# Kernel tuning notes

Measured on AMD Instinct MI355X. Metric: run time of the kernel, lower is better.

Reference implementation:

```python
import jax, jax.numpy as jnp
import numpy as np

D_MODEL = 1024
N_HEADS = 16
HEAD_DIM = D_MODEL // N_HEADS
L = 2048


def setup_inputs() -> dict:
    key = jax.random.key(0)
    ks = jax.random.split(key, 7)
    x = jax.random.normal(ks[0], (L, D_MODEL), dtype=jnp.float32)
    pair_bias = jax.random.normal(ks[1], (N_HEADS, L, L), dtype=jnp.float32)
    gate = jax.random.uniform(ks[2], (N_HEADS, 1, 1), dtype=jnp.float32)
    # Learned params (Linear stores weight [out, in]; y = x @ W.T + b)
    s_qkv = 1.0 / np.sqrt(D_MODEL)
    W_qkv = jax.random.uniform(ks[3], (3 * D_MODEL, D_MODEL), minval=-s_qkv, maxval=s_qkv, dtype=jnp.float32)
    b_qkv = jax.random.uniform(ks[4], (3 * D_MODEL,), minval=-s_qkv, maxval=s_qkv, dtype=jnp.float32)
    W_out = jax.random.uniform(ks[5], (D_MODEL, D_MODEL), minval=-s_qkv, maxval=s_qkv, dtype=jnp.float32)
    b_out = jax.random.uniform(ks[6], (D_MODEL,), minval=-s_qkv, maxval=s_qkv, dtype=jnp.float32)
    return {"x": x, "pair_bias": pair_bias, "gate": gate,
            "W_qkv": W_qkv, "b_qkv": b_qkv, "W_out": W_out, "b_out": b_out}


def reference(x, pair_bias, gate, W_qkv, b_qkv, W_out, b_out):
    Lx = x.shape[0]
    scale = HEAD_DIM ** -0.5
    qkv = (x @ W_qkv.T + b_qkv).reshape(Lx, 3, N_HEADS, HEAD_DIM)
    q, k, v = qkv[:, 0], qkv[:, 1], qkv[:, 2]  # [L, H, Dh]
    logits = jnp.einsum('ihd,jhd->hij', q, k) * scale + gate * pair_bias
    attn = jax.nn.softmax(logits, axis=-1)  # dropout p=0 (eval) -> identity
    out = jnp.einsum('hij,jhd->ihd', attn, v).reshape(Lx, D_MODEL)
    return out @ W_out.T + b_out
```

## Files before the change

### kernel.cpp

```cpp
#include <hip/hip_runtime.h>
#include <cstdint>
#include <cstddef>

#define L_SEQ  2048
#define DMODEL 1024
#define NHEADS 16
#define HDIM   64
#define NQKV   3072

typedef float f32x4 __attribute__((ext_vector_type(4)));
typedef short s16x8 __attribute__((ext_vector_type(8)));

static __device__ __forceinline__ unsigned short f2bf(float f) {
  unsigned u = __float_as_uint(f);
  return (unsigned short)((u + 0x7fffu + ((u >> 16) & 1u)) >> 16);
}

static __device__ __forceinline__ void gld_lds16(void* lds, const void* g) {
  __builtin_amdgcn_global_load_lds(
      (const __attribute__((address_space(1))) void*)g,
      (__attribute__((address_space(3))) void*)lds, 16, 0, 0);
}

__global__ __launch_bounds__(256) void cvt_kernel(
    const float* __restrict__ x, const float* __restrict__ wqkv,
    const float* __restrict__ wout,
    unsigned short* __restrict__ xb, unsigned short* __restrict__ wqkvb,
    unsigned short* __restrict__ woutb) {
  const int NX = L_SEQ * DMODEL / 4;
  const int NW1 = NQKV * DMODEL / 4;
  const int NW2 = DMODEL * DMODEL / 4;
  const int tot = NX + NW1 + NW2;
  for (int i = blockIdx.x * blockDim.x + threadIdx.x; i < tot;
       i += gridDim.x * blockDim.x) {
    const float4* s;
    unsigned short* d;
    int j;
    if (i < NX) { s = (const float4*)x; d = xb; j = i; }
    else if (i < NX + NW1) { s = (const float4*)wqkv; d = wqkvb; j = i - NX; }
    else { s = (const float4*)wout; d = woutb; j = i - NX - NW1; }
    float4 v = s[j];
    ushort4 o;
    o.x = f2bf(v.x); o.y = f2bf(v.y); o.z = f2bf(v.z); o.w = f2bf(v.w);
    *(ushort4*)(d + 4 * (size_t)j) = o;
  }
}

template <int KDIM>
static __device__ __forceinline__ void gemm_bt_core(
    const unsigned short* __restrict__ A, const unsigned short* __restrict__ Bt,
    unsigned short* As, unsigned short* Bs, int bm, int bn, f32x4 acc[4][4]) {
  const int tid = threadIdx.x;
  const int lane = tid & 63;
  const int wave = tid >> 6;
  const int g = lane >> 4;
  const int li = lane & 15;
  const int wm = (wave >> 1) * 64;
  const int wn = (wave & 1) * 64;
  const int arow = tid >> 2;
  const int acolb = (tid & 3) << 4;
  const char* gA = (const char*)A + (size_t)(bm * 128 + arow) * (KDIM * 2) + acolb;
  const char* gB = (const char*)Bt + (size_t)(bn * 128 + arow) * (KDIM * 2) + acolb;
  char* lA = (char*)As + wave * 1024;
  char* lB = (char*)Bs + wave * 1024;
  const size_t half = (size_t)64 * KDIM * 2;
  for (int kt = 0; kt < KDIM; kt += 32) {
    __syncthreads();
    gld_lds16(lA, gA + kt * 2);
    gld_lds16(lA + 4096, gA + half + kt * 2);
    gld_lds16(lB, gB + kt * 2);
    gld_lds16(lB + 4096, gB + half + kt * 2);
    __syncthreads();
    const s16x8* Av = (const s16x8*)As;
    const s16x8* Bv = (const s16x8*)Bs;
    s16x8 af[4], bfv[4];
#pragma unroll
    for (int mt = 0; mt < 4; ++mt) af[mt] = Av[(wm + mt * 16 + li) * 4 + g];
#pragma unroll
    for (int nt = 0; nt < 4; ++nt) bfv[nt] = Bv[(wn + nt * 16 + li) * 4 + g];
#pragma unroll
    for (int mt = 0; mt < 4; ++mt)
#pragma unroll
      for (int nt = 0; nt < 4; ++nt)
        acc[mt][nt] = __builtin_amdgcn_mfma_f32_16x16x32_bf16(
            af[mt], bfv[nt], acc[mt][nt], 0, 0, 0);
  }
}

__global__ __launch_bounds__(256, 2) void gemm_qkv_k(
    const unsigned short* __restrict__ A, const unsigned short* __restrict__ Bt,
    const float* __restrict__ bqkv, unsigned short* __restrict__ Qb,
    unsigned short* __restrict__ Kb, unsigned short* __restrict__ Vt) {
  __shared__ alignas(16) unsigned short As[128 * 32], Bs[128 * 32];
  f32x4 acc[4][4] = {};
  gemm_bt_core<DMODEL>(A, Bt, As, Bs, blockIdx.x, blockIdx.y, acc);
  const int lane = threadIdx.x & 63, wave = threadIdx.x >> 6;
  const int g = lane >> 4, li = lane & 15;
  const int wm = (wave >> 1) * 64, wn = (wave & 1) * 64;
#pragma unroll
  for (int mt = 0; mt < 4; ++mt)
#pragma unroll
    for (int nt = 0; nt < 4; ++nt)
#pragma unroll
      for (int r = 0; r < 4; ++r) {
        int i = blockIdx.x * 128 + wm + mt * 16 + 4 * g + r;
        int n = blockIdx.y * 128 + wn + nt * 16 + li;
        float v = acc[mt][nt][r] + bqkv[n];
        int s = n >> 10;
        int h = (n >> 6) & 15;
        int d = n & 63;
        if (s == 0)      Qb[(((size_t)h * L_SEQ + i) << 6) + d] = f2bf(v * 0.125f);
        else if (s == 1) Kb[(((size_t)h * L_SEQ + i) << 6) + d] = f2bf(v);
        else             Vt[(size_t)(h * 64 + d) * L_SEQ + i] = f2bf(v);
      }
}

__global__ __launch_bounds__(256, 4) void attn_k(
    const unsigned short* __restrict__ Qb, const unsigned short* __restrict__ Kb,
    const unsigned short* __restrict__ Vt, const float* __restrict__ bias,
    const float* __restrict__ gate, unsigned short* __restrict__ AO) {
  __shared__ alignas(16) char lds[16 * 1024 + 256];
  const int h = blockIdx.y;
  const int tid = threadIdx.x, lane = tid & 63, wave = tid >> 6;
  const int g = lane >> 4, li = lane & 15;
  const int i0 = blockIdx.x * 16;
  char* myP = lds + wave * 2048;
  const s16x8* Qv = (const s16x8*)(Qb + (((size_t)h * L_SEQ + i0) << 6));
  const s16x8 qf0 = Qv[li * 8 + g];
  const s16x8 qf1 = Qv[li * 8 + 4 + g];
  const float gh = gate[h];
  const float* bh = bias + (size_t)h * L_SEQ * L_SEQ + (size_t)i0 * L_SEQ;
  f32x4 accO[4] = {};
  f32x4 lpart = {0.f, 0.f, 0.f, 0.f};

  for (int t = 0; t < 8; ++t) {
    const int j0 = t * 256 + wave * 64;
    const s16x8* Kv = (const s16x8*)(Kb + (((size_t)h * L_SEQ + j0) << 6));
    s16x8 k0[4], k1[4];
#pragma unroll
    for (int nt = 0; nt < 4; ++nt) {
      k0[nt] = Kv[(nt * 16 + li) * 8 + g];
      k1[nt] = Kv[(nt * 16 + li) * 8 + 4 + g];
    }
    float bv[4][4];
#pragma unroll
    for (int r = 0; r < 4; ++r)
#pragma unroll
      for (int nt = 0; nt < 4; ++nt)
        bv[r][nt] = bh[(size_t)(4 * g + r) * L_SEQ + j0 + nt * 16 + li];
    f32x4 s[4];
#pragma unroll
    for (int nt = 0; nt < 4; ++nt) {
      f32x4 z = {0.f, 0.f, 0.f, 0.f};
      z = __builtin_amdgcn_mfma_f32_16x16x32_bf16(qf0, k0[nt], z, 0, 0, 0);
      z = __builtin_amdgcn_mfma_f32_16x16x32_bf16(qf1, k1[nt], z, 0, 0, 0);
      s[nt] = z;
    }
#pragma unroll
    for (int nt = 0; nt < 4; ++nt)
#pragma unroll
      for (int r = 0; r < 4; ++r) {
        float p = __expf(fmaf(gh, bv[r][nt], s[nt][r]));
        lpart[r] += p;
        int row = 4 * g + r, col = nt * 16 + li;
        unsigned b = (unsigned)(row * 128 + col * 2) ^ (unsigned)((row & 7) << 4);
        *(unsigned short*)(myP + b) = f2bf(p);
      }
    asm volatile("s_waitcnt lgkmcnt(0)" ::: "memory");
    unsigned b0 = ((unsigned)(li * 128 + 16 * g)) ^ (unsigned)((li & 7) << 4);
    unsigned b1 = ((unsigned)(li * 128 + 64 + 16 * g)) ^ (unsigned)((li & 7) << 4);
    s16x8 pa0 = *(const s16x8*)(myP + b0);
    s16x8 pa1 = *(const s16x8*)(myP + b1);
#pragma unroll
    for (int dt = 0; dt < 4; ++dt) {
      size_t vb = (size_t)(h * 64 + dt * 16 + li) * L_SEQ + j0;
      s16x8 v0 = *(const s16x8*)(Vt + vb + 8 * g);
      s16x8 v1 = *(const s16x8*)(Vt + vb + 32 + 8 * g);
      accO[dt] = __builtin_amdgcn_mfma_f32_16x16x32_bf16(pa0, v0, accO[dt], 0, 0, 0);
      accO[dt] = __builtin_amdgcn_mfma_f32_16x16x32_bf16(pa1, v1, accO[dt], 0, 0, 0);
    }
  }
  float lrow[4];
#pragma unroll
  for (int r = 0; r < 4; ++r) {
    float tl = lpart[r];
    tl += __shfl_xor(tl, 1);
    tl += __shfl_xor(tl, 2);
    tl += __shfl_xor(tl, 4);
    tl += __shfl_xor(tl, 8);
    lrow[r] = tl;
  }
  __syncthreads();
  float* accL = (float*)lds;
  float* lL = (float*)(lds + 16 * 1024);
#pragma unroll
  for (int dt = 0; dt < 4; ++dt)
#pragma unroll
    for (int r = 0; r < 4; ++r)
      accL[(wave * 16 + 4 * g + r) * 64 + dt * 16 + li] = accO[dt][r];
  if (li == 0) {
#pragma unroll
    for (int r = 0; r < 4; ++r) lL[wave * 16 + 4 * g + r] = lrow[r];
  }
  __syncthreads();
  {
    const int row = tid >> 4;
    const int c0 = (tid & 15) * 4;
    f32x4 sum = {0.f, 0.f, 0.f, 0.f};
    float lsum = 0.f;
#pragma unroll
    for (int w = 0; w < 4; ++w) {
      const f32x4 a = *(const f32x4*)&accL[(w * 16 + row) * 64 + c0];
      sum += a;
      lsum += lL[w * 16 + row];
    }
    const float inv = 1.0f / lsum;
    ushort4 o;
    o.x = f2bf(sum[0] * inv);
    o.y = f2bf(sum[1] * inv);
    o.z = f2bf(sum[2] * inv);
    o.w = f2bf(sum[3] * inv);
    *(ushort4*)(AO + (size_t)(i0 + row) * DMODEL + h * 64 + c0) = o;
  }
}

__global__ __launch_bounds__(256, 2) void gemm_out_k(
    const unsigned short* __restrict__ A, const unsigned short* __restrict__ Bt,
    const float* __restrict__ bout, float* __restrict__ out) {
  __shared__ alignas(16) unsigned short As[128 * 32], Bs[128 * 32];
  f32x4 acc[4][4] = {};
  gemm_bt_core<DMODEL>(A, Bt, As, Bs, blockIdx.x, blockIdx.y, acc);
  const int lane = threadIdx.x & 63, wave = threadIdx.x >> 6;
  const int g = lane >> 4, li = lane & 15;
  const int wm = (wave >> 1) * 64, wn = (wave & 1) * 64;
#pragma unroll
  for (int mt = 0; mt < 4; ++mt)
#pragma unroll
    for (int nt = 0; nt < 4; ++nt)
#pragma unroll
      for (int r = 0; r < 4; ++r) {
        int i = blockIdx.x * 128 + wm + mt * 16 + 4 * g + r;
        int n = blockIdx.y * 128 + wn + nt * 16 + li;
        out[(size_t)i * DMODEL + n] = acc[mt][nt][r] + bout[n];
      }
}

extern "C" void kernel_launch(void* const* d_in, const int* in_sizes, int n_in,
                              void* d_out, int out_size, void* d_ws,
                              size_t ws_size, hipStream_t stream) {
  const float* x = (const float*)d_in[0];
  const float* pb = (const float*)d_in[1];
  const float* gate = (const float*)d_in[2];
  const float* wqkv = (const float*)d_in[3];
  const float* bqkv = (const float*)d_in[4];
  const float* wout = (const float*)d_in[5];
  const float* bout = (const float*)d_in[6];

  unsigned short* ws = (unsigned short*)d_ws;
  unsigned short* xb = ws;
  unsigned short* wqkvb = xb + (size_t)L_SEQ * DMODEL;
  unsigned short* woutb = wqkvb + (size_t)NQKV * DMODEL;
  unsigned short* Qb = woutb + (size_t)DMODEL * DMODEL;
  unsigned short* Kb = Qb + (size_t)NHEADS * L_SEQ * HDIM;
  unsigned short* Vt = Kb + (size_t)NHEADS * L_SEQ * HDIM;
  unsigned short* AO = Vt + (size_t)NHEADS * L_SEQ * HDIM;

  cvt_kernel<<<1024, 256, 0, stream>>>(x, wqkv, wout, xb, wqkvb, woutb);
  gemm_qkv_k<<<dim3(16, 24), 256, 0, stream>>>(xb, wqkvb, bqkv, Qb, Kb, Vt);
  attn_k<<<dim3(128, 16), 256, 0, stream>>>(Qb, Kb, Vt, pb, gate, AO);
  gemm_out_k<<<dim3(16, 8), 256, 0, stream>>>(AO, woutb, bout, (float*)d_out);
}
```

Before: 204.6 us.

## Software-pipeline K and bias loads in attention loop with register double buffering

Prefetches the next iteration's K fragments and pair-bias values into double-buffered registers while the current tile computes, and hoists V loads to the top of each iteration. The aim is to hide global-memory latency on the bias stream, which dominates traffic. The loop is fully unrolled and occupancy is lowered from 4 to 2 blocks per SIMD in launch bounds to make room for the extra registers. That trades latency hiding through more waves for latency hiding through explicit prefetch.

```diff
diff --git a/kernel.cpp b/kernel.cpp
--- a/kernel.cpp
+++ b/kernel.cpp
@@ -115,7 +115,7 @@
       }
 }
 
-__global__ __launch_bounds__(256, 4) void attn_k(
+__global__ __launch_bounds__(256, 2) void attn_k(
     const unsigned short* __restrict__ Qb, const unsigned short* __restrict__ Kb,
     const unsigned short* __restrict__ Vt, const float* __restrict__ bias,
     const float* __restrict__ gate, unsigned short* __restrict__ AO) {
@@ -130,37 +130,68 @@
   const s16x8 qf1 = Qv[li * 8 + 4 + g];
   const float gh = gate[h];
   const float* bh = bias + (size_t)h * L_SEQ * L_SEQ + (size_t)i0 * L_SEQ;
+  const s16x8* Kall = (const s16x8*)(Kb + (((size_t)h * L_SEQ) << 6));
   f32x4 accO[4] = {};
   f32x4 lpart = {0.f, 0.f, 0.f, 0.f};
 
+  s16x8 kf[2][8];
+  float bb[2][16];
+
+  {
+    const int j0 = wave * 64;
+#pragma unroll
+    for (int nt = 0; nt < 4; ++nt) {
+      kf[0][2 * nt] = Kall[(j0 + nt * 16 + li) * 8 + g];
+      kf[0][2 * nt + 1] = Kall[(j0 + nt * 16 + li) * 8 + 4 + g];
+    }
+#pragma unroll
+    for (int r = 0; r < 4; ++r)
+#pragma unroll
+      for (int nt = 0; nt < 4; ++nt)
+        bb[0][4 * r + nt] = bh[(size_t)(4 * g + r) * L_SEQ + j0 + nt * 16 + li];
+  }
+
+#pragma unroll
   for (int t = 0; t < 8; ++t) {
+    const int cb = t & 1, nb = cb ^ 1;
     const int j0 = t * 256 + wave * 64;
-    const s16x8* Kv = (const s16x8*)(Kb + (((size_t)h * L_SEQ + j0) << 6));
-    s16x8 k0[4], k1[4];
-#pragma unroll
-    for (int nt = 0; nt < 4; ++nt) {
-      k0[nt] = Kv[(nt * 16 + li) * 8 + g];
-      k1[nt] = Kv[(nt * 16 + li) * 8 + 4 + g];
-    }
-    float bv[4][4];
-#pragma unroll
-    for (int r = 0; r < 4; ++r)
-#pragma unroll
-      for (int nt = 0; nt < 4; ++nt)
-        bv[r][nt] = bh[(size_t)(4 * g + r) * L_SEQ + j0 + nt * 16 + li];
+    s16x8 v0[4], v1[4];
+#pragma unroll
+    for (int dt = 0; dt < 4; ++dt) {
+      const unsigned short* vb = Vt + (size_t)(h * 64 + dt * 16 + li) * L_SEQ + j0;
+      v0[dt] = *(const s16x8*)(vb + 8 * g);
+      v1[dt] = *(const s16x8*)(vb + 32 + 8 * g);
+    }
+    if (t < 7) {
+      const int jn = j0 + 256;
+#pragma unroll
+      for (int r = 0; r < 4; ++r)
+#pragma unroll
+        for (int nt = 0; nt < 4; ++nt)
+          bb[nb][4 * r + nt] =
+              bh[(size_t)(4 * g + r) * L_SEQ + jn + nt * 16 + li];
+    }
     f32x4 s[4];
 #pragma unroll
     for (int nt = 0; nt < 4; ++nt) {
       f32x4 z = {0.f, 0.f, 0.f, 0.f};
-      z = __builtin_amdgcn_mfma_f32_16x16x32_bf16(qf0, k0[nt], z, 0, 0, 0);
-      z = __builtin_amdgcn_mfma_f32_16x16x32_bf16(qf1, k1[nt], z, 0, 0, 0);
+      z = __builtin_amdgcn_mfma_f32_16x16x32_bf16(qf0, kf[cb][2 * nt], z, 0, 0, 0);
+      z = __builtin_amdgcn_mfma_f32_16x16x32_bf16(qf1, kf[cb][2 * nt + 1], z, 0, 0, 0);
       s[nt] = z;
     }
+    if (t < 7) {
+      const int jn = j0 + 256;
+#pragma unroll
+      for (int nt = 0; nt < 4; ++nt) {
+        kf[nb][2 * nt] = Kall[(jn + nt * 16 + li) * 8 + g];
+        kf[nb][2 * nt + 1] = Kall[(jn + nt * 16 + li) * 8 + 4 + g];
+      }
+    }
 #pragma unroll
     for (int nt = 0; nt < 4; ++nt)
 #pragma unroll
       for (int r = 0; r < 4; ++r) {
-        float p = __expf(fmaf(gh, bv[r][nt], s[nt][r]));
+        float p = __expf(fmaf(gh, bb[cb][4 * r + nt], s[nt][r]));
         lpart[r] += p;
         int row = 4 * g + r, col = nt * 16 + li;
         unsigned b = (unsigned)(row * 128 + col * 2) ^ (unsigned)((row & 7) << 4);
@@ -173,11 +204,8 @@
     s16x8 pa1 = *(const s16x8*)(myP + b1);
 #pragma unroll
     for (int dt = 0; dt < 4; ++dt) {
-      size_t vb = (size_t)(h * 64 + dt * 16 + li) * L_SEQ + j0;
-      s16x8 v0 = *(const s16x8*)(Vt + vb + 8 * g);
-      s16x8 v1 = *(const s16x8*)(Vt + vb + 32 + 8 * g);
-      accO[dt] = __builtin_amdgcn_mfma_f32_16x16x32_bf16(pa0, v0, accO[dt], 0, 0, 0);
-      accO[dt] = __builtin_amdgcn_mfma_f32_16x16x32_bf16(pa1, v1, accO[dt], 0, 0, 0);
+      accO[dt] = __builtin_amdgcn_mfma_f32_16x16x32_bf16(pa0, v0[dt], accO[dt], 0, 0, 0);
+      accO[dt] = __builtin_amdgcn_mfma_f32_16x16x32_bf16(pa1, v1[dt], accO[dt], 0, 0, 0);
     }
   }
   float lrow[4];
```

Result: faster. 191.0 us (-6.7%).

## Split attention into score kernel writing exp scores and separate PV kernel

Applied to the files above, without the earlier changes.

Splits the fused attention kernel into two. The first computes exp(QK^T + gate*bias) for every tile in parallel across a 3D grid and stores bf16 probabilities to a global buffer. The second reads those probabilities, sums them for normalization, and multiplies them by V. This exposes more parallelism for the bias-streaming stage but adds a large global round trip of the full score matrix and needs extra workspace.

```diff
diff --git a/kernel.cpp b/kernel.cpp
--- a/kernel.cpp
+++ b/kernel.cpp
@@ -14,6 +14,10 @@
 static __device__ __forceinline__ unsigned short f2bf(float f) {
   unsigned u = __float_as_uint(f);
   return (unsigned short)((u + 0x7fffu + ((u >> 16) & 1u)) >> 16);
+}
+
+static __device__ __forceinline__ float bf2f(unsigned short u) {
+  return __uint_as_float(((unsigned)u) << 16);
 }
 
 static __device__ __forceinline__ void gld_lds16(void* lds, const void* g) {
@@ -115,82 +119,92 @@
       }
 }
 
-__global__ __launch_bounds__(256, 4) void attn_k(
+__global__ __launch_bounds__(256) void attn_score_k(
     const unsigned short* __restrict__ Qb, const unsigned short* __restrict__ Kb,
-    const unsigned short* __restrict__ Vt, const float* __restrict__ bias,
-    const float* __restrict__ gate, unsigned short* __restrict__ AO) {
-  __shared__ alignas(16) char lds[16 * 1024 + 256];
-  const int h = blockIdx.y;
+    const float* __restrict__ bias, const float* __restrict__ gate,
+    unsigned short* __restrict__ E) {
+  __shared__ alignas(16) char plds[4 * 2048];
+  const int h = blockIdx.z;
+  const int i0 = blockIdx.x * 16;
   const int tid = threadIdx.x, lane = tid & 63, wave = tid >> 6;
   const int g = lane >> 4, li = lane & 15;
-  const int i0 = blockIdx.x * 16;
-  char* myP = lds + wave * 2048;
+  const int j0 = blockIdx.y * 256 + wave * 64;
+  char* myP = plds + wave * 2048;
   const s16x8* Qv = (const s16x8*)(Qb + (((size_t)h * L_SEQ + i0) << 6));
   const s16x8 qf0 = Qv[li * 8 + g];
   const s16x8 qf1 = Qv[li * 8 + 4 + g];
   const float gh = gate[h];
-  const float* bh = bias + (size_t)h * L_SEQ * L_SEQ + (size_t)i0 * L_SEQ;
+  const float* bh = bias + (size_t)h * L_SEQ * L_SEQ + (size_t)i0 * L_SEQ + j0;
+  const s16x8* Kv = (const s16x8*)(Kb + (((size_t)h * L_SEQ + j0) << 6));
+  s16x8 k0[4], k1[4];
+#pragma unroll
+  for (int nt = 0; nt < 4; ++nt) {
+    k0[nt] = Kv[(nt * 16 + li) * 8 + g];
+    k1[nt] = Kv[(nt * 16 + li) * 8 + 4 + g];
+  }
+  float bv[4][4];
+#pragma unroll
+  for (int r = 0; r < 4; ++r)
+#pragma unroll
+    for (int nt = 0; nt < 4; ++nt)
+      bv[r][nt] = bh[(size_t)(4 * g + r) * L_SEQ + nt * 16 + li];
+  f32x4 s[4];
+#pragma unroll
+  for (int nt = 0; nt < 4; ++nt) {
+    f32x4 z = {0.f, 0.f, 0.f, 0.f};
+    z = __builtin_amdgcn_mfma_f32_16x16x32_bf16(qf0, k0[nt], z, 0, 0, 0);
+    z = __builtin_amdgcn_mfma_f32_16x16x32_bf16(qf1, k1[nt], z, 0, 0, 0);
+    s[nt] = z;
+  }
+#pragma unroll
+  for (int nt = 0; nt < 4; ++nt)
+#pragma unroll
+    for (int r = 0; r < 4; ++r) {
+      float p = __expf(fmaf(gh, bv[r][nt], s[nt][r]));
+      const int row = 4 * g + r, col = nt * 16 + li;
+      unsigned b = (unsigned)(row * 128 + col * 2) ^ (unsigned)((row & 7) << 4);
+      *(unsigned short*)(myP + b) = f2bf(p);
+    }
+  asm volatile("s_waitcnt lgkmcnt(0)" ::: "memory");
+  const unsigned b0 = ((unsigned)(li * 128 + 16 * g)) ^ (unsigned)((li & 7) << 4);
+  const unsigned b1 = ((unsigned)(li * 128 + 64 + 16 * g)) ^ (unsigned)((li & 7) << 4);
+  const s16x8 pa0 = *(const s16x8*)(myP + b0);
+  const s16x8 pa1 = *(const s16x8*)(myP + b1);
+  unsigned short* Eo = E + ((size_t)h * L_SEQ + (i0 + li)) * L_SEQ + j0 + 8 * g;
+  *(s16x8*)Eo = pa0;
+  *(s16x8*)(Eo + 32) = pa1;
+}
+
+__global__ __launch_bounds__(256) void attn_pv_k(
+    const unsigned short* __restrict__ E, const unsigned short* __restrict__ Vt,
+    unsigned short* __restrict__ AO) {
+  __shared__ alignas(16) char lds[16 * 1024 + 256];
+  const int h = blockIdx.y;
+  const int tid = threadIdx.x, lane = tid & 63, wave = tid >> 6;
+  const int g = lane >> 4, li = lane & 15;
+  const int i0 = blockIdx.x * 16;
+  const unsigned short* Eb = E + ((size_t)h * L_SEQ + (i0 + li)) * L_SEQ;
   f32x4 accO[4] = {};
-  f32x4 lpart = {0.f, 0.f, 0.f, 0.f};
-
+  float lsum = 0.f;
+#pragma unroll
   for (int t = 0; t < 8; ++t) {
     const int j0 = t * 256 + wave * 64;
-    const s16x8* Kv = (const s16x8*)(Kb + (((size_t)h * L_SEQ + j0) << 6));
-    s16x8 k0[4], k1[4];
-#pragma unroll
-    for (int nt = 0; nt < 4; ++nt) {
-      k0[nt] = Kv[(nt * 16 + li) * 8 + g];
-      k1[nt] = Kv[(nt * 16 + li) * 8 + 4 + g];
-    }
-    float bv[4][4];
-#pragma unroll
-    for (int r = 0; r < 4; ++r)
-#pragma unroll
-      for (int nt = 0; nt < 4; ++nt)
-        bv[r][nt] = bh[(size_t)(4 * g + r) * L_SEQ + j0 + nt * 16 + li];
-    f32x4 s[4];
-#pragma unroll
-    for (int nt = 0; nt < 4; ++nt) {
-      f32x4 z = {0.f, 0.f, 0.f, 0.f};
-      z = __builtin_amdgcn_mfma_f32_16x16x32_bf16(qf0, k0[nt], z, 0, 0, 0);
-      z = __builtin_amdgcn_mfma_f32_16x16x32_bf16(qf1, k1[nt], z, 0, 0, 0);
-      s[nt] = z;
-    }
-#pragma unroll
-    for (int nt = 0; nt < 4; ++nt)
-#pragma unroll
-      for (int r = 0; r < 4; ++r) {
-        float p = __expf(fmaf(gh, bv[r][nt], s[nt][r]));
-        lpart[r] += p;
-        int row = 4 * g + r, col = nt * 16 + li;
-        unsigned b = (unsigned)(row * 128 + col * 2) ^ (unsigned)((row & 7) << 4);
-        *(unsigned short*)(myP + b) = f2bf(p);
-      }
-    asm volatile("s_waitcnt lgkmcnt(0)" ::: "memory");
-    unsigned b0 = ((unsigned)(li * 128 + 16 * g)) ^ (unsigned)((li & 7) << 4);
-    unsigned b1 = ((unsigned)(li * 128 + 64 + 16 * g)) ^ (unsigned)((li & 7) << 4);
-    s16x8 pa0 = *(const s16x8*)(myP + b0);
-    s16x8 pa1 = *(const s16x8*)(myP + b1);
+    const s16x8 pa0 = *(const s16x8*)(Eb + j0 + 8 * g);
+    const s16x8 pa1 = *(const s16x8*)(Eb + j0 + 32 + 8 * g);
+#pragma unroll
+    for (int e = 0; e < 8; ++e)
+      lsum += bf2f((unsigned short)pa0[e]) + bf2f((unsigned short)pa1[e]);
 #pragma unroll
     for (int dt = 0; dt < 4; ++dt) {
-      size_t vb = (size_t)(h * 64 + dt * 16 + li) * L_SEQ + j0;
-      s16x8 v0 = *(const s16x8*)(Vt + vb + 8 * g);
-      s16x8 v1 = *(const s16x8*)(Vt + vb + 32 + 8 * g);
+      const unsigned short* vb = Vt + (size_t)(h * 64 + dt * 16 + li) * L_SEQ + j0;
+      const s16x8 v0 = *(const s16x8*)(vb + 8 * g);
+      const s16x8 v1 = *(const s16x8*)(vb + 32 + 8 * g);
       accO[dt] = __builtin_amdgcn_mfma_f32_16x16x32_bf16(pa0, v0, accO[dt], 0, 0, 0);
       accO[dt] = __builtin_amdgcn_mfma_f32_16x16x32_bf16(pa1, v1, accO[dt], 0, 0, 0);
     }
   }
-  float lrow[4];
-#pragma unroll
-  for (int r = 0; r < 4; ++r) {
-    float tl = lpart[r];
-    tl += __shfl_xor(tl, 1);
-    tl += __shfl_xor(tl, 2);
-    tl += __shfl_xor(tl, 4);
-    tl += __shfl_xor(tl, 8);
-    lrow[r] = tl;
-  }
-  __syncthreads();
+  lsum += __shfl_xor(lsum, 16);
+  lsum += __shfl_xor(lsum, 32);
   float* accL = (float*)lds;
   float* lL = (float*)(lds + 16 * 1024);
 #pragma unroll
@@ -198,23 +212,20 @@
 #pragma unroll
     for (int r = 0; r < 4; ++r)
       accL[(wave * 16 + 4 * g + r) * 64 + dt * 16 + li] = accO[dt][r];
-  if (li == 0) {
-#pragma unroll
-    for (int r = 0; r < 4; ++r) lL[wave * 16 + 4 * g + r] = lrow[r];
-  }
+  if (lane < 16) lL[wave * 16 + lane] = lsum;
   __syncthreads();
   {
     const int row = tid >> 4;
     const int c0 = (tid & 15) * 4;
     f32x4 sum = {0.f, 0.f, 0.f, 0.f};
-    float lsum = 0.f;
+    float ls = 0.f;
 #pragma unroll
     for (int w = 0; w < 4; ++w) {
       const f32x4 a = *(const f32x4*)&accL[(w * 16 + row) * 64 + c0];
       sum += a;
-      lsum += lL[w * 16 + row];
+      ls += lL[w * 16 + row];
     }
-    const float inv = 1.0f / lsum;
+    const float inv = 1.0f / ls;
     ushort4 o;
     o.x = f2bf(sum[0] * inv);
     o.y = f2bf(sum[1] * inv);
@@ -264,9 +275,11 @@
   unsigned short* Kb = Qb + (size_t)NHEADS * L_SEQ * HDIM;
   unsigned short* Vt = Kb + (size_t)NHEADS * L_SEQ * HDIM;
   unsigned short* AO = Vt + (size_t)NHEADS * L_SEQ * HDIM;
+  unsigned short* E  = AO + (size_t)L_SEQ * DMODEL;
 
   cvt_kernel<<<1024, 256, 0, stream>>>(x, wqkv, wout, xb, wqkvb, woutb);
   gemm_qkv_k<<<dim3(16, 24), 256, 0, stream>>>(xb, wqkvb, bqkv, Qb, Kb, Vt);
-  attn_k<<<dim3(128, 16), 256, 0, stream>>>(Qb, Kb, Vt, pb, gate, AO);
+  attn_score_k<<<dim3(128, 8, 16), 256, 0, stream>>>(Qb, Kb, pb, gate, E);
+  attn_pv_k<<<dim3(128, 16), 256, 0, stream>>>(E, Vt, AO);
   gemm_out_k<<<dim3(16, 8), 256, 0, stream>>>(AO, woutb, bout, (float*)d_out);
 }
```

Result: slower. 267.4 us (+30.7%).
